# Optimization experiments

Measured on AMD Instinct MI355X. Metric: run time of the kernel, lower is better.

## Reference

```python
import jax, jax.numpy as jnp
import numpy as np

C = 512

def conv1x1(x, w, b):
    # x: [B,C,H,W], w: [O,C], b: [O]
    return jnp.einsum('bchw,oc->bohw', x, w) + b[None, :, None, None]

def setup_inputs() -> dict:
    key = jax.random.key(0)
    ks = jax.random.split(key, 7)
    s = 1.0 / np.sqrt(C)
    x = jax.random.normal(ks[0], (8, C, 64, 64), dtype=jnp.float32)
    wq = jax.random.uniform(ks[1], (C, C), jnp.float32, -s, s)
    bq = jax.random.uniform(ks[2], (C,), jnp.float32, -s, s)
    wk = jax.random.uniform(ks[3], (C, C), jnp.float32, -s, s)
    bk = jax.random.uniform(ks[4], (C,), jnp.float32, -s, s)
    wv = jax.random.uniform(ks[5], (C, C), jnp.float32, -s, s)
    bv = jax.random.uniform(ks[6], (C,), jnp.float32, -s, s)
    return {"x": x, "wq": wq, "bq": bq, "wk": wk, "bk": bk, "wv": wv, "bv": bv}

def reference(x, wq, bq, wk, bk, wv, bv):
    B, Cc, H, W = x.shape
    q = conv1x1(x, wq, bq).reshape(B, Cc, H * W)   # [B,C,N]
    k = conv1x1(x, wk, bk).reshape(B, Cc, H * W)   # [B,C,N]
    v = conv1x1(x, wv, bv).reshape(B, Cc, H * W)   # [B,C,N]
    attn = jnp.einsum('bcn,bdn->bcd', q, k)        # q @ k^T over spatial dim -> [B,C,C]
    attn = jax.nn.softmax(attn, axis=-1)
    out = jnp.einsum('bcd,bdn->bcn', attn, v).reshape(B, Cc, H, W)
    return out + x
```

## Files before the change

### kernel.cpp

```cpp
#include <hip/hip_runtime.h>
#include <cstdint>

typedef unsigned short u16;
typedef unsigned int   u32;
typedef _Float16 f16;

typedef __attribute__((ext_vector_type(8))) _Float16 f16x8;
typedef __attribute__((ext_vector_type(4))) float    f32x4;

__device__ __forceinline__ u16 f2h(float f) {
    union { f16 h; u16 u; } c; c.h = (f16)f; return c.u;
}
__device__ __forceinline__ float h2f(u16 u) {
    union { u16 u; f16 h; } c; c.u = u; return (float)c.h;
}

__device__ __forceinline__ void async_copy16(const u16* g, u16* lds) {
    __builtin_amdgcn_global_load_lds(
        (const __attribute__((address_space(1))) void*)g,
        (__attribute__((address_space(3))) void*)lds,
        16, 0, 0);
}

__device__ __forceinline__ void gemm_nt_f16(
    u16* smem, const u16* __restrict__ A, int lda,
    const u16* __restrict__ B, int ldb, int K, f32x4 acc[4][4])
{
    const int t = threadIdx.x, w = t >> 6, lane = t & 63;
    const int srow = lane >> 2;
    const int skc  = (((lane & 3) ^ ((lane >> 3) & 3)) * 8);
    const int ra0 = (w*2+0)*16 + srow, ra1 = (w*2+1)*16 + srow;
    const u16* gA0 = A + (size_t)ra0 * lda + skc;
    const u16* gA1 = A + (size_t)ra1 * lda + skc;
    const u16* gB0 = B + (size_t)ra0 * ldb + skc;
    const u16* gB1 = B + (size_t)ra1 * ldb + skc;
    u16* lA0 = smem + (w*2+0)*512;
    u16* lA1 = smem + (w*2+1)*512;
    const int fr = lane & 15, fq = lane >> 4;
    const int fc = (fq ^ ((fr >> 1) & 3)) * 8;
    const int wm = (w >> 1) * 64, wn = (w & 1) * 64;
    const int fAo = (wm + fr) * 32 + fc;
    const int fBo = (wn + fr) * 32 + fc;

    for (int k0 = 0; k0 < K; k0 += 64) {
        async_copy16(gA0 + k0,      lA0);
        async_copy16(gA1 + k0,      lA1);
        async_copy16(gA0 + k0 + 32, lA0 + 4096);
        async_copy16(gA1 + k0 + 32, lA1 + 4096);
        async_copy16(gB0 + k0,      lA0 + 8192);
        async_copy16(gB1 + k0,      lA1 + 8192);
        async_copy16(gB0 + k0 + 32, lA0 + 12288);
        async_copy16(gB1 + k0 + 32, lA1 + 12288);
        __syncthreads();
        {
            f16x8 af[4], bf[4];
#pragma unroll
            for (int i = 0; i < 4; i++) af[i] = *(const f16x8*)(smem + fAo + i * 512);
#pragma unroll
            for (int i = 0; i < 4; i++) bf[i] = *(const f16x8*)(smem + 8192 + fBo + i * 512);
#pragma unroll
            for (int mi = 0; mi < 4; mi++)
#pragma unroll
                for (int ni = 0; ni < 4; ni++)
                    acc[mi][ni] = __builtin_amdgcn_mfma_f32_16x16x32_f16(
                        af[mi], bf[ni], acc[mi][ni], 0, 0, 0);
        }
        {
            f16x8 af[4], bf[4];
#pragma unroll
            for (int i = 0; i < 4; i++) af[i] = *(const f16x8*)(smem + 4096 + fAo + i * 512);
#pragma unroll
            for (int i = 0; i < 4; i++) bf[i] = *(const f16x8*)(smem + 12288 + fBo + i * 512);
#pragma unroll
            for (int mi = 0; mi < 4; mi++)
#pragma unroll
                for (int ni = 0; ni < 4; ni++)
                    acc[mi][ni] = __builtin_amdgcn_mfma_f32_16x16x32_f16(
                        af[mi], bf[ni], acc[mi][ni], 0, 0, 0);
        }
        __syncthreads();
    }
}

__device__ __forceinline__ void zero_acc(f32x4 acc[4][4]) {
#pragma unroll
    for (int i = 0; i < 4; i++)
#pragma unroll
        for (int j = 0; j < 4; j++) {
            f32x4 z = {0.f, 0.f, 0.f, 0.f};
            acc[i][j] = z;
        }
}

__global__ __launch_bounds__(256) void k_prep(const float* __restrict__ wq,
                                              const float* __restrict__ wk,
                                              const float* __restrict__ wv,
                                              u16* __restrict__ Wq2,
                                              u16* __restrict__ Wkh,
                                              u16* __restrict__ WvT,
                                              float* __restrict__ s)
{
    if (blockIdx.x < 512) {
        const int t = blockIdx.x * 256 + threadIdx.x;
        if (t < 4096) s[t] = 0.f;
        const int e = t * 4;
        const int sel = e >> 18;
        const int off = e & 262143;
        const float* src = sel ? wk : wq;
        float4 v = *(const float4*)(src + off);
        ushort4 h;
        h.x = f2h(v.x); h.y = f2h(v.y); h.z = f2h(v.z); h.w = f2h(v.w);
        if (sel == 0) {
            int i = off >> 9, c = off & 511;
            *(ushort4*)(Wq2 + (size_t)i * 1024 + c) = h;
            *(ushort4*)(Wq2 + (size_t)i * 1024 + 512 + c) = h;
        } else {
            *(ushort4*)(Wkh + off) = h;
        }
    } else {
        __shared__ u16 tile[64][70];
        const int bx = blockIdx.x - 512;
        const int t = threadIdx.x;
        const int d0 = (bx >> 3) * 64;
        const int c0 = (bx & 7) * 64;
        const int rr = t >> 4, col4 = (t & 15) * 4;
#pragma unroll
        for (int i = 0; i < 4; i++) {
            int row = i * 16 + rr;
            float4 v = *(const float4*)(wv + (size_t)(d0 + row) * 512 + c0 + col4);
            ushort4 h;
            h.x = f2h(v.x); h.y = f2h(v.y); h.z = f2h(v.z); h.w = f2h(v.w);
            *(ushort4*)&tile[row][col4] = h;
        }
        __syncthreads();
#pragma unroll
        for (int i = 0; i < 4; i++) {
            int crow = i * 16 + rr;
            ushort4 o;
            o.x = tile[col4 + 0][crow];
            o.y = tile[col4 + 1][crow];
            o.z = tile[col4 + 2][crow];
            o.w = tile[col4 + 3][crow];
            *(ushort4*)(WvT + (size_t)(c0 + crow) * 512 + d0 + col4) = o;
        }
    }
}

__global__ __launch_bounds__(256) void k_convx(const float* __restrict__ x,
                                               u16* __restrict__ Xh,
                                               u16* __restrict__ XT,
                                               float* __restrict__ s)
{
    __shared__ u16 tile[64][70];
    const int t  = threadIdx.x;
    const int b  = blockIdx.z;
    const int c0 = blockIdx.y * 64;
    const int n0 = blockIdx.x * 64;
    const int rr   = t >> 4;
    const int col4 = (t & 15) * 4;

    const float* src = x + ((size_t)b * 512 + c0) * 4096 + n0;
    u16* xh = Xh + ((size_t)b * 512 + c0) * 4096 + n0;
#pragma unroll
    for (int i = 0; i < 4; i++) {
        int row = i * 16 + rr;
        float4 v = *(const float4*)(src + (size_t)row * 4096 + col4);
        ushort4 h;
        h.x = f2h(v.x); h.y = f2h(v.y); h.z = f2h(v.z); h.w = f2h(v.w);
        *(ushort4*)&tile[row][col4] = h;
        *(ushort4*)(xh + (size_t)row * 4096 + col4) = h;
        float p = v.x + v.y + v.z + v.w;
        p += __shfl_xor(p, 1); p += __shfl_xor(p, 2);
        p += __shfl_xor(p, 4); p += __shfl_xor(p, 8);
        if ((t & 15) == 0) atomicAdd(&s[b * 512 + c0 + row], p);
    }
    __syncthreads();
    u16* dst = XT + ((size_t)b * 4096 + n0) * 512 + c0;
#pragma unroll
    for (int i = 0; i < 4; i++) {
        int nrow = i * 16 + rr;
        ushort4 o;
        o.x = tile[col4 + 0][nrow];
        o.y = tile[col4 + 1][nrow];
        o.z = tile[col4 + 2][nrow];
        o.w = tile[col4 + 3][nrow];
        *(ushort4*)(dst + (size_t)nrow * 512 + col4) = o;
    }
}

__global__ __launch_bounds__(256, 4) void k_gram(const u16* __restrict__ Xh,
                                                 float* __restrict__ Gp)
{
    __shared__ u16 smem[16384];
    const int n0 = blockIdx.x * 128;
    const int m0 = blockIdx.y * 128;
    const int bz = blockIdx.z;
    const int b  = bz >> 2, ks = bz & 3;

    const u16* Ap = Xh + (size_t)b * 512 * 4096 + (size_t)m0 * 4096 + ks * 1024;
    const u16* Bp = Xh + (size_t)b * 512 * 4096 + (size_t)n0 * 4096 + ks * 1024;

    f32x4 acc[4][4];
    zero_acc(acc);
    gemm_nt_f16(smem, Ap, 4096, Bp, 4096, 1024, acc);

    const int t = threadIdx.x, w = t >> 6, lane = t & 63;
    const int wm = (w >> 1) * 64, wn = (w & 1) * 64;
    const int cn = lane & 15, cq = lane >> 4;

    float* outp = Gp + ((size_t)(ks * 8 + b) * 512 + m0) * 512 + n0;
#pragma unroll
    for (int mi = 0; mi < 4; mi++)
#pragma unroll
        for (int ni = 0; ni < 4; ni++)
#pragma unroll
            for (int r = 0; r < 4; r++) {
                int m = wm + mi * 16 + cq * 4 + r;
                int n = wn + ni * 16 + cn;
                outp[(size_t)m * 512 + n] = acc[mi][ni][r];
            }
}

__global__ __launch_bounds__(256) void k_gred(const float* __restrict__ Gp,
                                              u16* __restrict__ Ghl,
                                              const float* __restrict__ wq,
                                              const float* __restrict__ bq,
                                              const float* __restrict__ wk,
                                              const float* __restrict__ s,
                                              float* __restrict__ ubar,
                                              float* __restrict__ vv)
{
    const size_t idx = ((size_t)blockIdx.x * 256 + threadIdx.x) * 4;
    const size_t st = (size_t)8 * 512 * 512;
    float4 g0 = *(const float4*)(Gp + idx);
    float4 g1 = *(const float4*)(Gp + idx + st);
    float4 g2 = *(const float4*)(Gp + idx + 2 * st);
    float4 g3 = *(const float4*)(Gp + idx + 3 * st);
    float gx = g0.x + g1.x + g2.x + g3.x;
    float gy = g0.y + g1.y + g2.y + g3.y;
    float gz = g0.z + g1.z + g2.z + g3.z;
    float gw = g0.w + g1.w + g2.w + g3.w;
    ushort4 hi, lo;
    hi.x = f2h(gx); lo.x = f2h(gx - h2f(hi.x));
    hi.y = f2h(gy); lo.y = f2h(gy - h2f(hi.y));
    hi.z = f2h(gz); lo.z = f2h(gz - h2f(hi.z));
    hi.w = f2h(gw); lo.w = f2h(gw - h2f(hi.w));
    const size_t row = idx >> 9;
    const int c = (int)(idx & 511);
    *(ushort4*)(Ghl + row * 1024 + c) = hi;
    *(ushort4*)(Ghl + row * 1024 + 512 + c) = lo;

    if (blockIdx.x < 128) {
        const int b = blockIdx.x >> 4;
        const int sub = blockIdx.x & 15;
        const int which = sub >> 3;
        const int r0 = (sub & 7) * 64;
        const int t = threadIdx.x;
        const int i = r0 + (t >> 2), l4 = t & 3;
        const float* W = which ? wk : wq;
        const float* sb = s + b * 512;
        float acc = 0.f;
#pragma unroll 4
        for (int k = 0; k < 32; k++) {
            int c2 = k * 16 + l4 * 4;
            float4 w4 = *(const float4*)(W + (size_t)i * 512 + c2);
            float4 s4 = *(const float4*)(sb + c2);
            acc += w4.x * s4.x + w4.y * s4.y + w4.z * s4.z + w4.w * s4.w;
        }
        acc += __shfl_xor(acc, 1);
        acc += __shfl_xor(acc, 2);
        if (l4 == 0) {
            if (which) vv[b * 512 + i] = acc;
            else       ubar[b * 512 + i] = acc + 4096.0f * bq[i];
        }
    }
}

__global__ __launch_bounds__(256, 4) void k_T(const u16* __restrict__ Wq2,
                                              const u16* __restrict__ Ghl,
                                              u16* __restrict__ Tb)
{
    __shared__ u16 smem[16384];
    const int n0 = blockIdx.x * 128;
    const int m0 = blockIdx.y * 128;
    const int b  = blockIdx.z;

    const u16* Ap = Wq2 + (size_t)m0 * 1024;
    const u16* Bp = Ghl + (size_t)b * 512 * 1024 + (size_t)n0 * 1024;

    f32x4 acc[4][4];
    zero_acc(acc);
    gemm_nt_f16(smem, Ap, 1024, Bp, 1024, 1024, acc);

    const int t = threadIdx.x, w = t >> 6, lane = t & 63;
    const int wm = (w >> 1) * 64, wn = (w & 1) * 64;
    const int cn = lane & 15, cq = lane >> 4;

    u16* outp = Tb + ((size_t)b * 512 + m0) * 512 + n0;
#pragma unroll
    for (int mi = 0; mi < 4; mi++)
#pragma unroll
        for (int ni = 0; ni < 4; ni++)
#pragma unroll
            for (int r = 0; r < 4; r++) {
                int m = wm + mi * 16 + cq * 4 + r;
                int n = wn + ni * 16 + cn;
                outp[(size_t)m * 512 + n] = f2h(acc[mi][ni][r]);
            }
}

__global__ __launch_bounds__(256) void k_S(
    const u16* __restrict__ Tb, const u16* __restrict__ Wkh,
    const float* __restrict__ ubar, const float* __restrict__ vv,
    const float* __restrict__ bq, const float* __restrict__ bk,
    const float* __restrict__ bv,
    u16* __restrict__ P, float* __restrict__ pbv)
{
    __shared__ u16 smem[16896];
    __shared__ float redm[16][4];
    __shared__ float reds[16][4][2];
    u16* As = smem; u16* Bs = smem + 512;

    const int m0 = blockIdx.x * 16;
    const int b  = blockIdx.y;
    const int t = threadIdx.x, w = t >> 6, lane = t & 63;
    const int srow = lane >> 2;
    const int schunk = ((lane & 3) ^ ((srow >> 1) & 3)) * 8;
    const u16* gA = Tb + ((size_t)b * 512 + m0 + srow) * 512 + schunk;
    const int fr = lane & 15, fq = lane >> 4;
    const int fc = (fq ^ ((fr >> 1) & 3)) * 8;

    f32x4 acc[8];
#pragma unroll
    for (int i = 0; i < 8; i++) { f32x4 z = {0.f,0.f,0.f,0.f}; acc[i] = z; }

    for (int k0 = 0; k0 < 512; k0 += 32) {
        if (w == 0) async_copy16(gA + k0, As);
#pragma unroll
        for (int ii = 0; ii < 8; ii++) {
            int rbase = w * 128 + ii * 16;
            async_copy16(Wkh + (size_t)(rbase + srow) * 512 + k0 + schunk,
                         Bs + rbase * 32);
        }
        __syncthreads();
        f16x8 af = *(const f16x8*)(As + fr * 32 + fc);
#pragma unroll
        for (int ni = 0; ni < 8; ni++) {
            f16x8 bf = *(const f16x8*)(Bs + (w * 128 + ni * 16 + fr) * 32 + fc);
            acc[ni] = __builtin_amdgcn_mfma_f32_16x16x32_f16(af, bf, acc[ni], 0, 0, 0);
        }
        __syncthreads();
    }

    const int cn = lane & 15, cq = lane >> 4;
    float ub[4], bqr[4];
#pragma unroll
    for (int r = 0; r < 4; r++) {
        int i = m0 + cq * 4 + r;
        ub[r]  = ubar[b * 512 + i];
        bqr[r] = bq[i];
    }
    float vj[8], bkj[8], bvj[8];
#pragma unroll
    for (int ni = 0; ni < 8; ni++) {
        int j = w * 128 + ni * 16 + cn;
        vj[ni]  = vv[b * 512 + j];
        bkj[ni] = bk[j];
        bvj[ni] = bv[j];
    }
    float sv[8][4], mr[4];
#pragma unroll
    for (int r = 0; r < 4; r++) mr[r] = -1e30f;
#pragma unroll
    for (int ni = 0; ni < 8; ni++)
#pragma unroll
        for (int r = 0; r < 4; r++) {
            sv[ni][r] = acc[ni][r] + ub[r] * bkj[ni] + bqr[r] * vj[ni];
            mr[r] = fmaxf(mr[r], sv[ni][r]);
        }
#pragma unroll
    for (int r = 0; r < 4; r++)
        for (int o = 1; o < 16; o <<= 1) mr[r] = fmaxf(mr[r], __shfl_xor(mr[r], o));
    if (cn == 0) {
#pragma unroll
        for (int r = 0; r < 4; r++) redm[cq * 4 + r][w] = mr[r];
    }
    __syncthreads();
#pragma unroll
    for (int r = 0; r < 4; r++) {
        int row = cq * 4 + r;
        mr[r] = fmaxf(fmaxf(redm[row][0], redm[row][1]),
                      fmaxf(redm[row][2], redm[row][3]));
    }
    float e[8][4], se[4], sebv[4];
#pragma unroll
    for (int r = 0; r < 4; r++) { se[r] = 0.f; sebv[r] = 0.f; }
#pragma unroll
    for (int ni = 0; ni < 8; ni++)
#pragma unroll
        for (int r = 0; r < 4; r++) {
            float ev = __expf(sv[ni][r] - mr[r]);
            e[ni][r] = ev;
            se[r]   += ev;
            sebv[r] += ev * bvj[ni];
        }
#pragma unroll
    for (int r = 0; r < 4; r++)
        for (int o = 1; o < 16; o <<= 1) {
            se[r]   += __shfl_xor(se[r], o);
            sebv[r] += __shfl_xor(sebv[r], o);
        }
    if (cn == 0) {
#pragma unroll
        for (int r = 0; r < 4; r++) {
            reds[cq * 4 + r][w][0] = se[r];
            reds[cq * 4 + r][w][1] = sebv[r];
        }
    }
    __syncthreads();
#pragma unroll
    for (int r = 0; r < 4; r++) {
        int row = cq * 4 + r;
        float S  = reds[row][0][0] + reds[row][1][0] + reds[row][2][0] + reds[row][3][0];
        float SB = reds[row][0][1] + reds[row][1][1] + reds[row][2][1] + reds[row][3][1];
        float inv = 1.0f / S;
#pragma unroll
        for (int ni = 0; ni < 8; ni++)
            P[((size_t)b * 512 + m0 + row) * 512 + w * 128 + ni * 16 + cn] =
                f2h(e[ni][r] * inv);
        if (w == 0 && cn == 0) pbv[b * 512 + m0 + row] = SB * inv;
    }
}

__global__ __launch_bounds__(256, 4) void k_M(const u16* __restrict__ P,
                                              const u16* __restrict__ WvT,
                                              u16* __restrict__ M2)
{
    __shared__ u16 smem[16384];
    const int n0 = blockIdx.x * 128;
    const int m0 = blockIdx.y * 128;
    const int b  = blockIdx.z;

    const u16* Ap = P + (size_t)b * 512 * 512 + (size_t)m0 * 512;
    const u16* Bp = WvT + (size_t)n0 * 512;

    f32x4 acc[4][4];
    zero_acc(acc);
    gemm_nt_f16(smem, Ap, 512, Bp, 512, 512, acc);

    const int t = threadIdx.x, w = t >> 6, lane = t & 63;
    const int wm = (w >> 1) * 64, wn = (w & 1) * 64;
    const int cn = lane & 15, cq = lane >> 4;

    u16* outp = M2 + ((size_t)b * 512 + m0) * 512 + n0;
#pragma unroll
    for (int mi = 0; mi < 4; mi++)
#pragma unroll
        for (int ni = 0; ni < 4; ni++)
#pragma unroll
            for (int r = 0; r < 4; r++) {
                int m = wm + mi * 16 + cq * 4 + r;
                int n = wn + ni * 16 + cn;
                outp[(size_t)m * 512 + n] = f2h(acc[mi][ni][r]);
            }
}

__global__ __launch_bounds__(256, 4) void k_out(const u16* __restrict__ M2,
                                                const u16* __restrict__ XT,
                                                const u16* __restrict__ Xh,
                                                const float* __restrict__ pbv,
                                                float* __restrict__ out)
{
    __shared__ u16 smem[16384];
    const int n0 = blockIdx.x * 128;
    const int m0 = blockIdx.y * 128;
    const int b  = blockIdx.z;

    const u16* Ap = M2 + (size_t)b * 512 * 512 + (size_t)m0 * 512;
    const u16* Bp = XT + (size_t)b * 4096 * 512 + (size_t)n0 * 512;

    f32x4 acc[4][4];
    zero_acc(acc);
    gemm_nt_f16(smem, Ap, 512, Bp, 512, 512, acc);

    const int t = threadIdx.x, w = t >> 6, lane = t & 63;
    const int wm = (w >> 1) * 64, wn = (w & 1) * 64;
    const int cn = lane & 15, cq = lane >> 4;

#pragma unroll
    for (int mi = 0; mi < 4; mi++)
#pragma unroll
        for (int ni = 0; ni < 4; ni++)
#pragma unroll
            for (int r = 0; r < 4; r++) {
                int m = m0 + wm + mi * 16 + cq * 4 + r;
                int n = n0 + wn + ni * 16 + cn;
                size_t idx = ((size_t)b * 512 + m) * 4096 + n;
                out[idx] = acc[mi][ni][r] + pbv[b * 512 + m] + h2f(Xh[idx]);
            }
}

extern "C" void kernel_launch(void* const* d_in, const int* in_sizes, int n_in,
                              void* d_out, int out_size, void* d_ws, size_t ws_size,
                              hipStream_t stream)
{
    const float* x  = (const float*)d_in[0];
    const float* wq = (const float*)d_in[1];
    const float* bq = (const float*)d_in[2];
    const float* wk = (const float*)d_in[3];
    const float* bk = (const float*)d_in[4];
    const float* wv = (const float*)d_in[5];
    const float* bv = (const float*)d_in[6];
    float* out = (float*)d_out;

    char* ws = (char*)d_ws;
    u16*   Wq2  = (u16*)(ws);
    u16*   Wkh  = (u16*)(ws + 1048576);
    u16*   WvT  = (u16*)(ws + 1572864);
    float* s    = (float*)(ws + 2097152);
    float* ubar = (float*)(ws + 2113536);
    float* vv   = (float*)(ws + 2129920);
    float* pbv  = (float*)(ws + 2146304);
    u16*   Xh   = (u16*)(ws + 2162688);
    u16*   XT   = (u16*)(ws + 35717120);
    float* Gp   = (float*)(ws + 69271552);
    u16*   Ghl  = (u16*)(ws + 102825984);
    u16*   Tb   = (u16*)(ws + 111214592);
    u16*   P    = (u16*)(ws + 115408896);
    u16*   M2   = (u16*)(ws + 119603200);

    k_prep<<<dim3(576), dim3(256), 0, stream>>>(wq, wk, wv, Wq2, Wkh, WvT, s);
    k_convx<<<dim3(64, 8, 8), dim3(256), 0, stream>>>(x, Xh, XT, s);
    k_gram<<<dim3(4, 4, 32), dim3(256), 0, stream>>>(Xh, Gp);
    k_gred<<<dim3(2048), dim3(256), 0, stream>>>(Gp, Ghl, wq, bq, wk, s, ubar, vv);
    k_T<<<dim3(4, 4, 8), dim3(256), 0, stream>>>(Wq2, Ghl, Tb);
    k_S<<<dim3(32, 8), dim3(256), 0, stream>>>(Tb, Wkh, ubar, vv, bq, bk, bv, P, pbv);
    k_M<<<dim3(4, 4, 8), dim3(256), 0, stream>>>(P, WvT, M2);
    k_out<<<dim3(32, 4, 8), dim3(256), 0, stream>>>(M2, XT, Xh, pbv, out);
}
```

Baseline: 255.3 us.

## Exploit Gram symmetry and fuse T, softmax, and PV GEMMs into one kernel

The Gram kernel now computes only upper-triangular 128x128 tiles (10 of 16) and writes each off-diagonal tile twice, once transposed, so less MFMA work is needed for the symmetric X·Xᵀ. The T, S/softmax and M GEMMs are merged into one kernel per 16-row strip. Intermediate T and P rows stay in swizzled LDS instead of going to global memory, which removes two launches and their round trips. The cost is that the fused kernel has only 256 blocks, each running three sequential GEMM loops (1024+512+512 K), so parallelism is lower than the old 128x128-tiled k_T and k_M grids.

```diff
diff --git a/kernel.cpp b/kernel.cpp
--- a/kernel.cpp
+++ b/kernel.cpp
@@ -192,9 +192,12 @@
                                                  float* __restrict__ Gp)
 {
     __shared__ u16 smem[16384];
-    const int n0 = blockIdx.x * 128;
-    const int m0 = blockIdx.y * 128;
-    const int bz = blockIdx.z;
+    const int tI = blockIdx.x;
+    const int tm = (tI >= 9) ? 3 : (tI >= 7) ? 2 : (tI >= 4) ? 1 : 0;
+    const int rs = (tm == 0) ? 0 : (tm == 1) ? 4 : (tm == 2) ? 7 : 9;
+    const int tn = tI - rs + tm;
+    const int m0 = tm * 128, n0 = tn * 128;
+    const int bz = blockIdx.y;
     const int b  = bz >> 2, ks = bz & 3;
 
     const u16* Ap = Xh + (size_t)b * 512 * 4096 + (size_t)m0 * 4096 + ks * 1024;
@@ -208,7 +211,8 @@
     const int wm = (w >> 1) * 64, wn = (w & 1) * 64;
     const int cn = lane & 15, cq = lane >> 4;
 
-    float* outp = Gp + ((size_t)(ks * 8 + b) * 512 + m0) * 512 + n0;
+    float* base = Gp + (size_t)(ks * 8 + b) * 512 * 512;
+    float* outp = base + (size_t)m0 * 512 + n0;
 #pragma unroll
     for (int mi = 0; mi < 4; mi++)
 #pragma unroll
@@ -219,6 +223,19 @@
                 int n = wn + ni * 16 + cn;
                 outp[(size_t)m * 512 + n] = acc[mi][ni][r];
             }
+    if (m0 != n0) {
+        float* outT = base + (size_t)n0 * 512 + m0;
+#pragma unroll
+        for (int mi = 0; mi < 4; mi++)
+#pragma unroll
+            for (int ni = 0; ni < 4; ni++) {
+                int mb = wm + mi * 16 + cq * 4;
+                int n  = wn + ni * 16 + cn;
+                float4 v4 = { acc[mi][ni][0], acc[mi][ni][1],
+                              acc[mi][ni][2], acc[mi][ni][3] };
+                *(float4*)(outT + (size_t)n * 512 + mb) = v4;
+            }
+    }
 }
 
 __global__ __launch_bounds__(256) void k_gred(const float* __restrict__ Gp,
@@ -276,66 +293,71 @@
     }
 }
 
-__global__ __launch_bounds__(256, 4) void k_T(const u16* __restrict__ Wq2,
-                                              const u16* __restrict__ Ghl,
-                                              u16* __restrict__ Tb)
-{
-    __shared__ u16 smem[16384];
-    const int n0 = blockIdx.x * 128;
-    const int m0 = blockIdx.y * 128;
-    const int b  = blockIdx.z;
-
-    const u16* Ap = Wq2 + (size_t)m0 * 1024;
-    const u16* Bp = Ghl + (size_t)b * 512 * 1024 + (size_t)n0 * 1024;
-
-    f32x4 acc[4][4];
-    zero_acc(acc);
-    gemm_nt_f16(smem, Ap, 1024, Bp, 1024, 1024, acc);
-
-    const int t = threadIdx.x, w = t >> 6, lane = t & 63;
-    const int wm = (w >> 1) * 64, wn = (w & 1) * 64;
-    const int cn = lane & 15, cq = lane >> 4;
-
-    u16* outp = Tb + ((size_t)b * 512 + m0) * 512 + n0;
-#pragma unroll
-    for (int mi = 0; mi < 4; mi++)
-#pragma unroll
-        for (int ni = 0; ni < 4; ni++)
-#pragma unroll
-            for (int r = 0; r < 4; r++) {
-                int m = wm + mi * 16 + cq * 4 + r;
-                int n = wn + ni * 16 + cn;
-                outp[(size_t)m * 512 + n] = f2h(acc[mi][ni][r]);
-            }
-}
-
-__global__ __launch_bounds__(256) void k_S(
-    const u16* __restrict__ Tb, const u16* __restrict__ Wkh,
+__global__ __launch_bounds__(256) void k_TSM(
+    const u16* __restrict__ Wq2, const u16* __restrict__ Ghl,
+    const u16* __restrict__ Wkh, const u16* __restrict__ WvT,
     const float* __restrict__ ubar, const float* __restrict__ vv,
     const float* __restrict__ bq, const float* __restrict__ bk,
     const float* __restrict__ bv,
-    u16* __restrict__ P, float* __restrict__ pbv)
-{
-    __shared__ u16 smem[16896];
+    u16* __restrict__ M2, float* __restrict__ pbv)
+{
+    __shared__ u16 smem[25088];
     __shared__ float redm[16][4];
     __shared__ float reds[16][4][2];
-    u16* As = smem; u16* Bs = smem + 512;
+    u16* Bs = smem;
+    u16* As = smem + 16384;
+    u16* Ts = smem + 16896;
 
     const int m0 = blockIdx.x * 16;
     const int b  = blockIdx.y;
     const int t = threadIdx.x, w = t >> 6, lane = t & 63;
     const int srow = lane >> 2;
     const int schunk = ((lane & 3) ^ ((srow >> 1) & 3)) * 8;
-    const u16* gA = Tb + ((size_t)b * 512 + m0 + srow) * 512 + schunk;
     const int fr = lane & 15, fq = lane >> 4;
     const int fc = (fq ^ ((fr >> 1) & 3)) * 8;
+    const int cn = lane & 15, cq = lane >> 4;
+
+    const u16* Ghl_b = Ghl + (size_t)b * 512 * 1024;
 
     f32x4 acc[8];
+
 #pragma unroll
     for (int i = 0; i < 8; i++) { f32x4 z = {0.f,0.f,0.f,0.f}; acc[i] = z; }
-
+    {
+        const u16* gA = Wq2 + (size_t)(m0 + srow) * 1024 + schunk;
+        for (int k0 = 0; k0 < 1024; k0 += 32) {
+            if (w == 0) async_copy16(gA + k0, As);
+#pragma unroll
+            for (int ii = 0; ii < 8; ii++) {
+                int rbase = w * 128 + ii * 16;
+                async_copy16(Ghl_b + (size_t)(rbase + srow) * 1024 + k0 + schunk,
+                             Bs + rbase * 32);
+            }
+            __syncthreads();
+            f16x8 af = *(const f16x8*)(As + fr * 32 + fc);
+#pragma unroll
+            for (int ni = 0; ni < 8; ni++) {
+                f16x8 bf = *(const f16x8*)(Bs + (w * 128 + ni * 16 + fr) * 32 + fc);
+                acc[ni] = __builtin_amdgcn_mfma_f32_16x16x32_f16(af, bf, acc[ni], 0, 0, 0);
+            }
+            __syncthreads();
+        }
+    }
+#pragma unroll
+    for (int ni = 0; ni < 8; ni++) {
+        const int d = w * 128 + ni * 16 + cn;
+        const int kc = d >> 5, lc = (d & 31) >> 3, dl = d & 7;
+#pragma unroll
+        for (int r = 0; r < 4; r++) {
+            int mr = cq * 4 + r;
+            Ts[kc * 512 + mr * 32 + ((lc ^ ((mr >> 1) & 3)) << 3) + dl]
+                = f2h(acc[ni][r]);
+        }
+    }
+
+#pragma unroll
+    for (int i = 0; i < 8; i++) { f32x4 z = {0.f,0.f,0.f,0.f}; acc[i] = z; }
     for (int k0 = 0; k0 < 512; k0 += 32) {
-        if (w == 0) async_copy16(gA + k0, As);
 #pragma unroll
         for (int ii = 0; ii < 8; ii++) {
             int rbase = w * 128 + ii * 16;
@@ -343,7 +365,7 @@
                          Bs + rbase * 32);
         }
         __syncthreads();
-        f16x8 af = *(const f16x8*)(As + fr * 32 + fc);
+        f16x8 af = *(const f16x8*)(Ts + (k0 >> 5) * 512 + fr * 32 + fc);
 #pragma unroll
         for (int ni = 0; ni < 8; ni++) {
             f16x8 bf = *(const f16x8*)(Bs + (w * 128 + ni * 16 + fr) * 32 + fc);
@@ -352,7 +374,6 @@
         __syncthreads();
     }
 
-    const int cn = lane & 15, cq = lane >> 4;
     float ub[4], bqr[4];
 #pragma unroll
     for (int r = 0; r < 4; r++) {
@@ -368,29 +389,29 @@
         bkj[ni] = bk[j];
         bvj[ni] = bv[j];
     }
-    float sv[8][4], mr[4];
-#pragma unroll
-    for (int r = 0; r < 4; r++) mr[r] = -1e30f;
+    float sv[8][4], mr4[4];
+#pragma unroll
+    for (int r = 0; r < 4; r++) mr4[r] = -1e30f;
 #pragma unroll
     for (int ni = 0; ni < 8; ni++)
 #pragma unroll
         for (int r = 0; r < 4; r++) {
             sv[ni][r] = acc[ni][r] + ub[r] * bkj[ni] + bqr[r] * vj[ni];
-            mr[r] = fmaxf(mr[r], sv[ni][r]);
+            mr4[r] = fmaxf(mr4[r], sv[ni][r]);
         }
 #pragma unroll
     for (int r = 0; r < 4; r++)
-        for (int o = 1; o < 16; o <<= 1) mr[r] = fmaxf(mr[r], __shfl_xor(mr[r], o));
+        for (int o = 1; o < 16; o <<= 1) mr4[r] = fmaxf(mr4[r], __shfl_xor(mr4[r], o));
     if (cn == 0) {
 #pragma unroll
-        for (int r = 0; r < 4; r++) redm[cq * 4 + r][w] = mr[r];
+        for (int r = 0; r < 4; r++) redm[cq * 4 + r][w] = mr4[r];
     }
     __syncthreads();
 #pragma unroll
     for (int r = 0; r < 4; r++) {
         int row = cq * 4 + r;
-        mr[r] = fmaxf(fmaxf(redm[row][0], redm[row][1]),
-                      fmaxf(redm[row][2], redm[row][3]));
+        mr4[r] = fmaxf(fmaxf(redm[row][0], redm[row][1]),
+                       fmaxf(redm[row][2], redm[row][3]));
     }
     float e[8][4], se[4], sebv[4];
 #pragma unroll
@@ -399,7 +420,7 @@
     for (int ni = 0; ni < 8; ni++)
 #pragma unroll
         for (int r = 0; r < 4; r++) {
-            float ev = __expf(sv[ni][r] - mr[r]);
+            float ev = __expf(sv[ni][r] - mr4[r]);
             e[ni][r] = ev;
             se[r]   += ev;
             sebv[r] += ev * bvj[ni];
@@ -418,51 +439,53 @@
         }
     }
     __syncthreads();
+    float inv4[4];
 #pragma unroll
     for (int r = 0; r < 4; r++) {
         int row = cq * 4 + r;
         float S  = reds[row][0][0] + reds[row][1][0] + reds[row][2][0] + reds[row][3][0];
         float SB = reds[row][0][1] + reds[row][1][1] + reds[row][2][1] + reds[row][3][1];
-        float inv = 1.0f / S;
-#pragma unroll
-        for (int ni = 0; ni < 8; ni++)
-            P[((size_t)b * 512 + m0 + row) * 512 + w * 128 + ni * 16 + cn] =
-                f2h(e[ni][r] * inv);
-        if (w == 0 && cn == 0) pbv[b * 512 + m0 + row] = SB * inv;
-    }
-}
-
-__global__ __launch_bounds__(256, 4) void k_M(const u16* __restrict__ P,
-                                              const u16* __restrict__ WvT,
-                                              u16* __restrict__ M2)
-{
-    __shared__ u16 smem[16384];
-    const int n0 = blockIdx.x * 128;
-    const int m0 = blockIdx.y * 128;
-    const int b  = blockIdx.z;
-
-    const u16* Ap = P + (size_t)b * 512 * 512 + (size_t)m0 * 512;
-    const u16* Bp = WvT + (size_t)n0 * 512;
-
-    f32x4 acc[4][4];
-    zero_acc(acc);
-    gemm_nt_f16(smem, Ap, 512, Bp, 512, 512, acc);
-
-    const int t = threadIdx.x, w = t >> 6, lane = t & 63;
-    const int wm = (w >> 1) * 64, wn = (w & 1) * 64;
-    const int cn = lane & 15, cq = lane >> 4;
-
-    u16* outp = M2 + ((size_t)b * 512 + m0) * 512 + n0;
-#pragma unroll
-    for (int mi = 0; mi < 4; mi++)
-#pragma unroll
-        for (int ni = 0; ni < 4; ni++)
-#pragma unroll
-            for (int r = 0; r < 4; r++) {
-                int m = wm + mi * 16 + cq * 4 + r;
-                int n = wn + ni * 16 + cn;
-                outp[(size_t)m * 512 + n] = f2h(acc[mi][ni][r]);
-            }
+        inv4[r] = 1.0f / S;
+        if (w == 0 && cn == 0) pbv[b * 512 + m0 + row] = SB * inv4[r];
+    }
+#pragma unroll
+    for (int ni = 0; ni < 8; ni++) {
+        const int j = w * 128 + ni * 16 + cn;
+        const int kc = j >> 5, lc = (j & 31) >> 3, jl = j & 7;
+#pragma unroll
+        for (int r = 0; r < 4; r++) {
+            int mr = cq * 4 + r;
+            Ts[kc * 512 + mr * 32 + ((lc ^ ((mr >> 1) & 3)) << 3) + jl]
+                = f2h(e[ni][r] * inv4[r]);
+        }
+    }
+
+#pragma unroll
+    for (int i = 0; i < 8; i++) { f32x4 z = {0.f,0.f,0.f,0.f}; acc[i] = z; }
+    for (int k0 = 0; k0 < 512; k0 += 32) {
+#pragma unroll
+        for (int ii = 0; ii < 8; ii++) {
+            int rbase = w * 128 + ii * 16;
+            async_copy16(WvT + (size_t)(rbase + srow) * 512 + k0 + schunk,
+                         Bs + rbase * 32);
+        }
+        __syncthreads();
+        f16x8 af = *(const f16x8*)(Ts + (k0 >> 5) * 512 + fr * 32 + fc);
+#pragma unroll
+        for (int ni = 0; ni < 8; ni++) {
+            f16x8 bf = *(const f16x8*)(Bs + (w * 128 + ni * 16 + fr) * 32 + fc);
+            acc[ni] = __builtin_amdgcn_mfma_f32_16x16x32_f16(af, bf, acc[ni], 0, 0, 0);
+        }
+        __syncthreads();
+    }
+#pragma unroll
+    for (int ni = 0; ni < 8; ni++)
+#pragma unroll
+        for (int r = 0; r < 4; r++) {
+            int mr = cq * 4 + r;
+            M2[((size_t)b * 512 + m0 + mr) * 512 + w * 128 + ni * 16 + cn]
+                = f2h(acc[ni][r]);
+        }
 }
 
 __global__ __launch_bounds__(256, 4) void k_out(const u16* __restrict__ M2,
@@ -525,16 +548,13 @@
     u16*   XT   = (u16*)(ws + 35717120);
     float* Gp   = (float*)(ws + 69271552);
     u16*   Ghl  = (u16*)(ws + 102825984);
-    u16*   Tb   = (u16*)(ws + 111214592);
-    u16*   P    = (u16*)(ws + 115408896);
-    u16*   M2   = (u16*)(ws + 119603200);
+    u16*   M2   = (u16*)(ws + 111214592);
 
     k_prep<<<dim3(576), dim3(256), 0, stream>>>(wq, wk, wv, Wq2, Wkh, WvT, s);
     k_convx<<<dim3(64, 8, 8), dim3(256), 0, stream>>>(x, Xh, XT, s);
-    k_gram<<<dim3(4, 4, 32), dim3(256), 0, stream>>>(Xh, Gp);
+    k_gram<<<dim3(10, 32), dim3(256), 0, stream>>>(Xh, Gp);
     k_gred<<<dim3(2048), dim3(256), 0, stream>>>(Gp, Ghl, wq, bq, wk, s, ubar, vv);
-    k_T<<<dim3(4, 4, 8), dim3(256), 0, stream>>>(Wq2, Ghl, Tb);
-    k_S<<<dim3(32, 8), dim3(256), 0, stream>>>(Tb, Wkh, ubar, vv, bq, bk, bv, P, pbv);
-    k_M<<<dim3(4, 4, 8), dim3(256), 0, stream>>>(P, WvT, M2);
+    k_TSM<<<dim3(32, 8), dim3(256), 0, stream>>>(Wq2, Ghl, Wkh, WvT, ubar, vv,
+                                                 bq, bk, bv, M2, pbv);
     k_out<<<dim3(32, 4, 8), dim3(256), 0, stream>>>(M2, XT, Xh, pbv, out);
 }
```

Result: slower. 265.0 us (+3.8%).

## Exploit Gram symmetry and add XCD-aware block swizzles to gram and output GEMMs

Applied to the files above, without the earlier changes.

The Gram kernel now computes only the upper-triangular 128x128 tiles (10 of 16 per batch/split) and writes the mirrored tile transposed, cutting its GEMM work by roughly a third. Both k_gram and k_out switch to a flat 1D grid with a stride-8 swizzle so consecutive blocks mapped to the same XCD share operands in L2. The transposed store of the off-diagonal tiles uses float4 writes with a strided pattern, which costs extra store traffic.

```diff
diff --git a/kernel.cpp b/kernel.cpp
--- a/kernel.cpp
+++ b/kernel.cpp
@@ -192,9 +192,14 @@
                                                  float* __restrict__ Gp)
 {
     __shared__ u16 smem[16384];
-    const int n0 = blockIdx.x * 128;
-    const int m0 = blockIdx.y * 128;
-    const int bz = blockIdx.z;
+    const int flat = blockIdx.x;
+    const int swz  = (flat & 7) * 40 + (flat >> 3);
+    const int tI = swz % 10;
+    const int bz = swz / 10;
+    const int tm = (tI >= 9) ? 3 : (tI >= 7) ? 2 : (tI >= 4) ? 1 : 0;
+    const int rs = (tm == 0) ? 0 : (tm == 1) ? 4 : (tm == 2) ? 7 : 9;
+    const int tn = tI - rs + tm;
+    const int m0 = tm * 128, n0 = tn * 128;
     const int b  = bz >> 2, ks = bz & 3;
 
     const u16* Ap = Xh + (size_t)b * 512 * 4096 + (size_t)m0 * 4096 + ks * 1024;
@@ -208,7 +213,8 @@
     const int wm = (w >> 1) * 64, wn = (w & 1) * 64;
     const int cn = lane & 15, cq = lane >> 4;
 
-    float* outp = Gp + ((size_t)(ks * 8 + b) * 512 + m0) * 512 + n0;
+    float* base = Gp + (size_t)(ks * 8 + b) * 512 * 512;
+    float* outp = base + (size_t)m0 * 512 + n0;
 #pragma unroll
     for (int mi = 0; mi < 4; mi++)
 #pragma unroll
@@ -219,6 +225,19 @@
                 int n = wn + ni * 16 + cn;
                 outp[(size_t)m * 512 + n] = acc[mi][ni][r];
             }
+    if (m0 != n0) {
+        float* outT = base + (size_t)n0 * 512 + m0;
+#pragma unroll
+        for (int mi = 0; mi < 4; mi++)
+#pragma unroll
+            for (int ni = 0; ni < 4; ni++) {
+                int mb = wm + mi * 16 + cq * 4;
+                int n  = wn + ni * 16 + cn;
+                float4 v4 = { acc[mi][ni][0], acc[mi][ni][1],
+                              acc[mi][ni][2], acc[mi][ni][3] };
+                *(float4*)(outT + (size_t)n * 512 + mb) = v4;
+            }
+    }
 }
 
 __global__ __launch_bounds__(256) void k_gred(const float* __restrict__ Gp,
@@ -472,9 +491,11 @@
                                                 float* __restrict__ out)
 {
     __shared__ u16 smem[16384];
-    const int n0 = blockIdx.x * 128;
-    const int m0 = blockIdx.y * 128;
-    const int b  = blockIdx.z;
+    const int flat = blockIdx.x;
+    const int swz  = (flat & 7) * 128 + (flat >> 3);
+    const int n0 = (swz & 31) * 128;
+    const int m0 = ((swz >> 5) & 3) * 128;
+    const int b  = swz >> 7;
 
     const u16* Ap = M2 + (size_t)b * 512 * 512 + (size_t)m0 * 512;
     const u16* Bp = XT + (size_t)b * 4096 * 512 + (size_t)n0 * 512;
@@ -531,10 +552,10 @@
 
     k_prep<<<dim3(576), dim3(256), 0, stream>>>(wq, wk, wv, Wq2, Wkh, WvT, s);
     k_convx<<<dim3(64, 8, 8), dim3(256), 0, stream>>>(x, Xh, XT, s);
-    k_gram<<<dim3(4, 4, 32), dim3(256), 0, stream>>>(Xh, Gp);
+    k_gram<<<dim3(320), dim3(256), 0, stream>>>(Xh, Gp);
     k_gred<<<dim3(2048), dim3(256), 0, stream>>>(Gp, Ghl, wq, bq, wk, s, ubar, vv);
     k_T<<<dim3(4, 4, 8), dim3(256), 0, stream>>>(Wq2, Ghl, Tb);
     k_S<<<dim3(32, 8), dim3(256), 0, stream>>>(Tb, Wkh, ubar, vv, bq, bk, bv, P, pbv);
     k_M<<<dim3(4, 4, 8), dim3(256), 0, stream>>>(P, WvT, M2);
-    k_out<<<dim3(32, 4, 8), dim3(256), 0, stream>>>(M2, XT, Xh, pbv, out);
-}
+    k_out<<<dim3(1024), dim3(256), 0, stream>>>(M2, XT, Xh, pbv, out);
+}
```

Result: faster. 250.0 us (-2.1%).
